# Kernel optimization log

Measured on AMD Instinct MI355X. Metric: run time of the kernel, lower is better.

The kernel has to match this reference:

```python
import jax, jax.numpy as jnp
import numpy as np

N_QUBITS = 10
DIM = 2 ** N_QUBITS
N_TOKENS = 32
LAYERS = 2
DEGREE = 3
VOCAB = 32000
EMB = 512
N_PARAMS = 4 * N_QUBITS * LAYERS      # angles per token circuit
N_PARAMS_FF = 4 * N_QUBITS            # quantum feedforward (1 layer)
BATCH = 32


def _ry(state, wire, theta, n):
    # state: [B, 2**n] complex64; theta: [B] float32. RY = [[c,-s],[s,c]], c=cos(th/2)
    st = state.reshape(-1, 2 ** wire, 2, 2 ** (n - wire - 1))
    c = jnp.cos(theta / 2)[:, None, None]
    s = jnp.sin(theta / 2)[:, None, None]
    a, b = st[:, :, 0, :], st[:, :, 1, :]
    st = jnp.stack([c * a - s * b, s * a + c * b], axis=2)
    return st.reshape(-1, 2 ** n)


def _crx(state, ctrl, tgt, theta, n):
    # controlled-RX: apply RX=[[c,-i s],[-i s,c]] on tgt where ctrl bit == 1
    lo, hi = (ctrl, tgt) if ctrl < tgt else (tgt, ctrl)
    st = state.reshape(-1, 2 ** lo, 2, 2 ** (hi - lo - 1), 2, 2 ** (n - hi - 1))
    caxis = 2 if ctrl < tgt else 4
    taxis = 4 if ctrl < tgt else 2
    c = jnp.cos(theta / 2).reshape(-1, 1, 1, 1, 1, 1)
    s = jnp.sin(theta / 2).reshape(-1, 1, 1, 1, 1, 1)
    c0 = jax.lax.index_in_dim(st, 0, caxis, keepdims=True)
    c1 = jax.lax.index_in_dim(st, 1, caxis, keepdims=True)
    a = jax.lax.index_in_dim(c1, 0, taxis, keepdims=True)
    b = jax.lax.index_in_dim(c1, 1, taxis, keepdims=True)
    na = c * a - 1j * s * b
    nb = -1j * s * a + c * b
    c1 = jnp.concatenate([na, nb], axis=taxis)
    st = jnp.concatenate([c0, c1], axis=caxis)
    return st.reshape(-1, 2 ** n)


def _ansatz14(state, params, n, layers):
    # gate order of ansatz 14 (arXiv:1905.10876); params: [B, 4*n*layers]
    idx = 0
    for _ in range(layers):
        for i in range(n):
            state = _ry(state, i, params[:, idx], n); idx += 1
        for i in range(n - 1, -1, -1):
            state = _crx(state, i, (i + 1) % n, params[:, idx], n); idx += 1
        for i in range(n):
            state = _ry(state, i, params[:, idx], n); idx += 1
        for i in [n - 1] + list(range(n - 1)):
            state = _crx(state, i, (i - 1) % n, params[:, idx], n); idx += 1
    return state


def _measure_xyz(state, n):
    # expectation of X,Y,Z on every wire; output [B, 3*n] ordered [x..., y..., z...]
    B = state.shape[0]
    xs, ys, zs = [], [], []
    for w in range(n):
        st = state.reshape(B, 2 ** w, 2, 2 ** (n - w - 1))
        a, b = st[:, :, 0, :], st[:, :, 1, :]
        z = jnp.sum(jnp.conj(a) * b, axis=(1, 2))
        xs.append(2.0 * jnp.real(z))
        ys.append(2.0 * jnp.imag(z))
        zs.append(jnp.sum(jnp.real(a * jnp.conj(a)) - jnp.real(b * jnp.conj(b)), axis=(1, 2)))
    return jnp.stack(xs + ys + zs, axis=1)


def _forward(x, emb, w_ang, b_ang, qsvt_coeffs, lcu_re, lcu_im, qff_params, w1, b1, w2, b2):
    B, T = x.shape
    lcu = (lcu_re + 1j * lcu_im).astype(jnp.complex64)
    lcu = lcu / jnp.maximum(jnp.sum(jnp.abs(lcu)), 1e-12)          # p=1 normalize
    angles = (emb[x] @ w_ang.T + b_ang).reshape(B * T, N_PARAMS)   # [B*T, P]
    init = jnp.zeros((B, DIM), jnp.complex64).at[:, 0].set(1.0)
    acc = qsvt_coeffs[0] * init
    mono = init
    for k in range(1, DEGREE + 1):
        rep = jnp.repeat(mono, T, axis=0)                          # [B*T, D]
        st = _ansatz14(rep, angles, N_QUBITS, LAYERS).reshape(B, T, DIM)
        mono = jnp.einsum('bwi,w->bi', st, lcu)                    # LCU combine
        acc = acc + qsvt_coeffs[k] * mono
    qsvt_state = acc / jnp.sum(jnp.abs(qsvt_coeffs))
    norm = jnp.linalg.norm(qsvt_state, axis=-1, keepdims=True)
    normed = qsvt_state / jnp.maximum(norm, 1e-12)
    qff = jnp.broadcast_to(qff_params[None, :], (B, N_PARAMS_FF))
    st2 = _ansatz14(normed, qff, N_QUBITS, 1)
    ev = _measure_xyz(st2, N_QUBITS)                               # [B, 3*nq]
    h = jax.nn.relu(ev @ w1.T + b1)
    logits = h @ w2.T + b2
    return logits, jnp.mean(norm[:, 0])


def setup_inputs() -> dict:
    key = jax.random.key(0)
    ks = jax.random.split(key, 9)
    return {
        'x': jax.random.randint(ks[0], (BATCH, N_TOKENS), 0, VOCAB, dtype=jnp.int32),
        'emb': jax.random.normal(ks[1], (VOCAB, EMB), jnp.float32) * 0.02,
        'w_ang': jax.random.normal(ks[2], (N_PARAMS, EMB), jnp.float32) * (1.0 / np.sqrt(EMB)),
        'b_ang': jnp.zeros((N_PARAMS,), jnp.float32),
        'qsvt_coeffs': jax.random.uniform(ks[3], (DEGREE + 1,), jnp.float32),
        'lcu_re': jax.random.uniform(ks[4], (N_TOKENS,), jnp.float32),
        'lcu_im': jax.random.uniform(ks[5], (N_TOKENS,), jnp.float32),
        'qff_params': jax.random.uniform(ks[6], (N_PARAMS_FF,), jnp.float32),
        'w1': jax.random.normal(ks[7], (EMB, 3 * N_QUBITS), jnp.float32) * (1.0 / np.sqrt(3 * N_QUBITS)),
        'b1': jnp.zeros((EMB,), jnp.float32),
        'w2': jax.random.normal(ks[8], (VOCAB, EMB), jnp.float32) * (1.0 / np.sqrt(EMB)),
        'b2': jnp.zeros((VOCAB,), jnp.float32),
    }


def reference(x, emb, w_ang, b_ang, qsvt_coeffs, lcu_re, lcu_im, qff_params, w1, b1, w2, b2):
    return _forward(x, emb, w_ang, b_ang, qsvt_coeffs, lcu_re, lcu_im, qff_params, w1, b1, w2, b2)
```

## Files before the change

### kernel.cpp

```cpp
#include <hip/hip_runtime.h>
#include <math.h>

#define DEV __device__ __forceinline__

namespace {

struct C2 { float x, y; };

constexpr size_t OFF_CS   = 0;
constexpr size_t OFF_QFF  = 163840;
constexpr size_t OFF_LCU  = 163920;
constexpr size_t OFF_DEN  = 163984;
constexpr size_t OFF_NRM  = 163988;
constexpr size_t OFF_MONO = 164096;
constexpr size_t OFF_ACC  = 229632;
constexpr size_t OFF_ST   = 295168;
constexpr size_t OFF_EV   = 2392320;
constexpr size_t OFF_H    = 2393280;


template<int P>
DEV void ry_gate(C2 v[16], int lane, float c, float s) {
  if constexpr (P >= 6) {
    constexpr int rm = 1 << (P - 6);
#pragma unroll
    for (int r = 0; r < 16; ++r) {
      if ((r & rm) == 0) {
        C2 a = v[r], b = v[r | rm];
        v[r].x      = fmaf(c, a.x, -s * b.x);
        v[r].y      = fmaf(c, a.y, -s * b.y);
        v[r | rm].x = fmaf(s, a.x,  c * b.x);
        v[r | rm].y = fmaf(s, a.y,  c * b.y);
      }
    }
  } else {
    constexpr int lm = 1 << P;
    float sg = (lane & lm) ? s : -s;
#pragma unroll
    for (int r = 0; r < 16; ++r) {
      float px = __shfl_xor(v[r].x, lm, 64);
      float py = __shfl_xor(v[r].y, lm, 64);
      v[r].x = fmaf(c, v[r].x, sg * px);
      v[r].y = fmaf(c, v[r].y, sg * py);
    }
  }
}

template<int PC, int PT>
DEV void crx_gate(C2 v[16], int lane, float c, float s) {
  if constexpr (PT >= 6) {
    constexpr int tm = 1 << (PT - 6);
#pragma unroll
    for (int r = 0; r < 16; ++r) {
      if ((r & tm) == 0) {
        if constexpr (PC >= 6) {
          constexpr int cm = 1 << (PC - 6);
          if ((r & cm) != 0) {
            C2 a = v[r], b = v[r | tm];
            v[r].x      = fmaf(c, a.x,  s * b.y);
            v[r].y      = fmaf(c, a.y, -s * b.x);
            v[r | tm].x = fmaf(c, b.x,  s * a.y);
            v[r | tm].y = fmaf(c, b.y, -s * a.x);
          }
        } else {
          constexpr int cl = 1 << PC;
          bool ct = (lane & cl) != 0;
          C2 a = v[r], b = v[r | tm];
          float nax = fmaf(c, a.x,  s * b.y);
          float nay = fmaf(c, a.y, -s * b.x);
          float nbx = fmaf(c, b.x,  s * a.y);
          float nby = fmaf(c, b.y, -s * a.x);
          v[r].x      = ct ? nax : a.x;
          v[r].y      = ct ? nay : a.y;
          v[r | tm].x = ct ? nbx : b.x;
          v[r | tm].y = ct ? nby : b.y;
        }
      }
    }
  } else {
    constexpr int tm = 1 << PT;
#pragma unroll
    for (int r = 0; r < 16; ++r) {
      if constexpr (PC >= 6) {
        constexpr int cm = 1 << (PC - 6);
        if ((r & cm) == 0) continue;
      }
      float px = __shfl_xor(v[r].x, tm, 64);
      float py = __shfl_xor(v[r].y, tm, 64);
      float nx = fmaf(c, v[r].x,  s * py);
      float ny = fmaf(c, v[r].y, -s * px);
      if constexpr (PC >= 6) {
        v[r].x = nx; v[r].y = ny;
      } else {
        constexpr int cl = 1 << PC;
        bool ct = (lane & cl) != 0;
        v[r].x = ct ? nx : v[r].x;
        v[r].y = ct ? ny : v[r].y;
      }
    }
  }
}

#define RYG(w, g)       ry_gate<9-(w)>(v, lane, cs[2*(g)], cs[2*(g)+1])
#define CRXG(cw, tw, g) crx_gate<9-(cw), 9-(tw)>(v, lane, cs[2*(g)], cs[2*(g)+1])

DEV void apply_layer(C2 v[16], int lane, const float* __restrict__ cs) {
  RYG(0,0); RYG(1,1); RYG(2,2); RYG(3,3); RYG(4,4);
  RYG(5,5); RYG(6,6); RYG(7,7); RYG(8,8); RYG(9,9);
  CRXG(9,0,10); CRXG(8,9,11); CRXG(7,8,12); CRXG(6,7,13); CRXG(5,6,14);
  CRXG(4,5,15); CRXG(3,4,16); CRXG(2,3,17); CRXG(1,2,18); CRXG(0,1,19);
  RYG(0,20); RYG(1,21); RYG(2,22); RYG(3,23); RYG(4,24);
  RYG(5,25); RYG(6,26); RYG(7,27); RYG(8,28); RYG(9,29);
  CRXG(9,8,30); CRXG(0,9,31); CRXG(1,0,32); CRXG(2,1,33); CRXG(3,2,34);
  CRXG(4,3,35); CRXG(5,4,36); CRXG(6,5,37); CRXG(7,6,38); CRXG(8,7,39);
}

template<int P>
DEV void measure_wire(const C2 v[16], int lane, float* ev, int w) {
  float x = 0.f, y = 0.f, z = 0.f;
  if constexpr (P >= 6) {
    constexpr int rm = 1 << (P - 6);
#pragma unroll
    for (int r = 0; r < 16; ++r) {
      if ((r & rm) == 0) {
        C2 a = v[r], b = v[r | rm];
        x += a.x*b.x + a.y*b.y;
        y += a.x*b.y - a.y*b.x;
        z += (a.x*a.x + a.y*a.y) - (b.x*b.x + b.y*b.y);
      }
    }
  } else {
    constexpr int lm = 1 << P;
#pragma unroll
    for (int r = 0; r < 16; ++r) {
      float px = __shfl_xor(v[r].x, lm, 64);
      float py = __shfl_xor(v[r].y, lm, 64);
      if ((lane & lm) == 0) {
        C2 a = v[r];
        x += a.x*px + a.y*py;
        y += a.x*py - a.y*px;
        z += (a.x*a.x + a.y*a.y) - (px*px + py*py);
      }
    }
  }
  for (int s = 1; s < 64; s <<= 1) {
    x += __shfl_xor(x, s, 64);
    y += __shfl_xor(y, s, 64);
    z += __shfl_xor(z, s, 64);
  }
  if (lane == 0) {
    ev[w]      = 2.f * x;
    ev[10 + w] = 2.f * y;
    ev[20 + w] = z;
  }
}

DEV void measure_all(const C2 v[16], int lane, float* ev) {
  measure_wire<9>(v, lane, ev, 0);
  measure_wire<8>(v, lane, ev, 1);
  measure_wire<7>(v, lane, ev, 2);
  measure_wire<6>(v, lane, ev, 3);
  measure_wire<5>(v, lane, ev, 4);
  measure_wire<4>(v, lane, ev, 5);
  measure_wire<3>(v, lane, ev, 6);
  measure_wire<2>(v, lane, ev, 7);
  measure_wire<1>(v, lane, ev, 8);
  measure_wire<0>(v, lane, ev, 9);
}


__global__ void k_init(float* __restrict__ ws, const float* __restrict__ coef,
                       const float* __restrict__ lr, const float* __restrict__ li,
                       const float* __restrict__ qff) {
  if (blockIdx.x == 0 && threadIdx.x < 64) {
    int lane = threadIdx.x;
    float re = 0.f, im = 0.f;
    if (lane < 32) { re = lr[lane]; im = li[lane]; }
    float tot = sqrtf(re * re + im * im);
    for (int s = 1; s < 64; s <<= 1) tot += __shfl_xor(tot, s, 64);
    float L = fmaxf(tot, 1e-12f);
    if (lane < 32) {
      ws[OFF_LCU + 2 * lane]     = re / L;
      ws[OFF_LCU + 2 * lane + 1] = im / L;
    }
    float dv = (lane < 4) ? fabsf(coef[lane]) : 0.f;
    for (int s = 1; s < 64; s <<= 1) dv += __shfl_xor(dv, s, 64);
    if (lane == 0) ws[OFF_DEN] = dv;
    if (lane < 40) {
      float th = 0.5f * qff[lane];
      ws[OFF_QFF + 2 * lane]     = cosf(th);
      ws[OFF_QFF + 2 * lane + 1] = sinf(th);
    }
  }
  int idx = blockIdx.x * 256 + threadIdx.x;
  float c0 = coef[0];
  bool z = (idx & 1023) == 0;
  float2* mono = (float2*)(ws + OFF_MONO);
  float2* acc  = (float2*)(ws + OFF_ACC);
  mono[idx] = make_float2(z ? 1.f : 0.f, 0.f);
  acc[idx]  = make_float2(z ? c0 : 0.f, 0.f);
}

__global__ __launch_bounds__(128) void k_angles(const int* __restrict__ x,
                                                const float* __restrict__ emb,
                                                const float* __restrict__ w_ang,
                                                const float* __restrict__ b_ang,
                                                float* __restrict__ ws) {
  __shared__ float4 e4[128];
  int tok = blockIdx.x;
  int tid = threadIdx.x;
  int row = x[tok];
  e4[tid] = ((const float4*)(emb + (size_t)row * 512))[tid];
  __syncthreads();
  if (tid < 80) {
    const float4* wr = (const float4*)(w_ang + (size_t)tid * 512);
    float acc = b_ang[tid];
#pragma unroll 4
    for (int j = 0; j < 128; ++j) {
      float4 w = wr[j];
      float4 e = e4[j];
      acc = fmaf(w.x, e.x, acc);
      acc = fmaf(w.y, e.y, acc);
      acc = fmaf(w.z, e.z, acc);
      acc = fmaf(w.w, e.w, acc);
    }
    float th = 0.5f * acc;
    ws[OFF_CS + (size_t)tok * 160 + 2 * tid]     = cosf(th);
    ws[OFF_CS + (size_t)tok * 160 + 2 * tid + 1] = sinf(th);
  }
}

__global__ __launch_bounds__(256) void k_evolve(float* __restrict__ ws) {
  __shared__ float cs_lds[640];
  int tid = threadIdx.x;
  const float* csg = ws + OFF_CS + (size_t)blockIdx.x * 640;
  for (int i = tid; i < 640; i += 256) cs_lds[i] = csg[i];
  __syncthreads();
  int wid = tid >> 6, lane = tid & 63;
  int state = blockIdx.x * 4 + wid;
  int b = state >> 5, t = state & 31;
  const float2* mono = (const float2*)(ws + OFF_MONO) + (size_t)b * 1024;
  C2 v[16];
#pragma unroll
  for (int r = 0; r < 16; ++r) {
    float2 m = mono[(r << 6) | lane];
    v[r].x = m.x; v[r].y = m.y;
  }
  const float* csw = &cs_lds[wid * 160];
#pragma unroll 1
  for (int l = 0; l < 2; ++l)
    apply_layer(v, lane, csw + l * 80);
  float2 w = ((const float2*)(ws + OFF_LCU))[t];
  float2* st = (float2*)(ws + OFF_ST) + (size_t)state * 1024;
#pragma unroll
  for (int r = 0; r < 16; ++r) {
    st[(r << 6) | lane] = make_float2(w.x * v[r].x - w.y * v[r].y,
                                      w.x * v[r].y + w.y * v[r].x);
  }
}

__global__ void k_reduce(float* __restrict__ ws, const float* __restrict__ coef, int k) {
  int idx = blockIdx.x * 256 + threadIdx.x;
  int b = idx >> 10, i = idx & 1023;
  const float2* st = (const float2*)(ws + OFF_ST) + (size_t)b * 32768 + i;
  float sx = 0.f, sy = 0.f;
#pragma unroll
  for (int t = 0; t < 32; ++t) {
    float2 vv = st[t * 1024];
    sx += vv.x; sy += vv.y;
  }
  float2* mono = (float2*)(ws + OFF_MONO);
  float2* acc  = (float2*)(ws + OFF_ACC);
  mono[idx] = make_float2(sx, sy);
  float ck = coef[k];
  float2 a = acc[idx];
  a.x = fmaf(ck, sx, a.x);
  a.y = fmaf(ck, sy, a.y);
  acc[idx] = a;
}

__global__ __launch_bounds__(64) void k_final(float* __restrict__ ws) {
  int lane = threadIdx.x;
  int b = blockIdx.x;
  const float2* acc = (const float2*)(ws + OFF_ACC) + (size_t)b * 1024;
  float invd = 1.f / ws[OFF_DEN];
  C2 v[16];
  float ssum = 0.f;
#pragma unroll
  for (int r = 0; r < 16; ++r) {
    float2 m = acc[(r << 6) | lane];
    v[r].x = m.x * invd; v[r].y = m.y * invd;
    ssum += v[r].x * v[r].x + v[r].y * v[r].y;
  }
  for (int s = 1; s < 64; s <<= 1) ssum += __shfl_xor(ssum, s, 64);
  float nrm = sqrtf(ssum);
  if (lane == 0) ws[OFF_NRM + b] = nrm;
  float sc = 1.f / fmaxf(nrm, 1e-12f);
#pragma unroll
  for (int r = 0; r < 16; ++r) { v[r].x *= sc; v[r].y *= sc; }
  apply_layer(v, lane, ws + OFF_QFF);
  measure_all(v, lane, ws + OFF_EV + b * 30);
}

__global__ void k_mlp1(float* __restrict__ ws, const float* __restrict__ w1,
                       const float* __restrict__ b1, float* __restrict__ out) {
  int idx = blockIdx.x * 256 + threadIdx.x;
  int b = idx >> 9, j = idx & 511;
  const float* ev = ws + OFF_EV + b * 30;
  const float* wr = w1 + (size_t)j * 30;
  float a = b1[j];
#pragma unroll
  for (int q = 0; q < 30; ++q) a = fmaf(ev[q], wr[q], a);
  ws[OFF_H + idx] = fmaxf(a, 0.f);
  if (idx == 0) {
    float s = 0.f;
    for (int i = 0; i < 32; ++i) s += ws[OFF_NRM + i];
    out[32000u * 32u] = s * (1.f / 32.f);
  }
}

__global__ __launch_bounds__(256) void k_logits(const float* __restrict__ ws,
                                                const float* __restrict__ w2,
                                                const float* __restrict__ b2,
                                                float* __restrict__ out) {
  __shared__ float4 hT[4096];
  int tid = threadIdx.x;
  const float4* hg = (const float4*)(ws + OFF_H);
#pragma unroll
  for (int p = 0; p < 16; ++p) {
    int idx = tid + p * 256;
    int m = idx >> 7, kf4 = idx & 127;
    hT[m * 128 + (kf4 ^ (m >> 3))] = hg[idx];
  }
  __syncthreads();

  int wv = tid >> 6, lane = tid & 63;
  int mg = lane & 3, nl = lane >> 2;
  int nbase = blockIdx.x * 128;
  float acc[8][8];
#pragma unroll
  for (int j = 0; j < 8; ++j)
#pragma unroll
    for (int mi = 0; mi < 8; ++mi) acc[j][mi] = 0.f;

  const float* wbase = w2 + (size_t)(nbase + nl * 8) * 512 + wv * 128;
  int kqb = wv * 32;
  for (int kf4 = 0; kf4 < 32; ++kf4) {
    int kcol = kqb + kf4;
    float4 h4[8];
#pragma unroll
    for (int mi = 0; mi < 8; ++mi) {
      int m = mg * 8 + mi;
      h4[mi] = hT[m * 128 + (kcol ^ mg)];
    }
#pragma unroll
    for (int j = 0; j < 8; ++j) {
      float4 w4 = *(const float4*)(wbase + (size_t)j * 512 + kf4 * 4);
#pragma unroll
      for (int mi = 0; mi < 8; ++mi) {
        acc[j][mi] = fmaf(w4.x, h4[mi].x, acc[j][mi]);
        acc[j][mi] = fmaf(w4.y, h4[mi].y, acc[j][mi]);
        acc[j][mi] = fmaf(w4.z, h4[mi].z, acc[j][mi]);
        acc[j][mi] = fmaf(w4.w, h4[mi].w, acc[j][mi]);
      }
    }
  }

  __syncthreads();
  if (wv != 0) {
    int r = wv - 1;
    float4* cb = hT + r * 1024 + lane * 16;
#pragma unroll
    for (int mi = 0; mi < 8; ++mi) {
#pragma unroll
      for (int jh = 0; jh < 2; ++jh) {
        int q = mi * 2 + jh;
        float4 vv = make_float4(acc[jh*4+0][mi], acc[jh*4+1][mi],
                                acc[jh*4+2][mi], acc[jh*4+3][mi]);
        cb[q ^ (lane & 15)] = vv;
      }
    }
  }
  __syncthreads();
  if (wv == 0) {
#pragma unroll
    for (int r = 0; r < 3; ++r) {
      const float4* cb = hT + r * 1024 + lane * 16;
#pragma unroll
      for (int mi = 0; mi < 8; ++mi) {
#pragma unroll
        for (int jh = 0; jh < 2; ++jh) {
          int q = mi * 2 + jh;
          float4 vv = cb[q ^ (lane & 15)];
          acc[jh*4+0][mi] += vv.x;
          acc[jh*4+1][mi] += vv.y;
          acc[jh*4+2][mi] += vv.z;
          acc[jh*4+3][mi] += vv.w;
        }
      }
    }
    float4 b2lo = *(const float4*)(b2 + nbase + nl * 8);
    float4 b2hi = *(const float4*)(b2 + nbase + nl * 8 + 4);
#pragma unroll
    for (int mi = 0; mi < 8; ++mi) {
      int m = mg * 8 + mi;
      float* orow = out + (size_t)m * 32000 + nbase + nl * 8;
      float4 lo = make_float4(acc[0][mi] + b2lo.x, acc[1][mi] + b2lo.y,
                              acc[2][mi] + b2lo.z, acc[3][mi] + b2lo.w);
      float4 hi = make_float4(acc[4][mi] + b2hi.x, acc[5][mi] + b2hi.y,
                              acc[6][mi] + b2hi.z, acc[7][mi] + b2hi.w);
      *(float4*)(orow)     = lo;
      *(float4*)(orow + 4) = hi;
    }
  }
}

}

extern "C" void kernel_launch(void* const* d_in, const int* in_sizes, int n_in,
                              void* d_out, int out_size, void* d_ws, size_t ws_size,
                              hipStream_t stream) {
  (void)in_sizes; (void)n_in; (void)out_size; (void)ws_size;
  const int*   x    = (const int*)d_in[0];
  const float* emb  = (const float*)d_in[1];
  const float* wang = (const float*)d_in[2];
  const float* bang = (const float*)d_in[3];
  const float* coef = (const float*)d_in[4];
  const float* lre  = (const float*)d_in[5];
  const float* lim  = (const float*)d_in[6];
  const float* qff  = (const float*)d_in[7];
  const float* w1   = (const float*)d_in[8];
  const float* b1   = (const float*)d_in[9];
  const float* w2   = (const float*)d_in[10];
  const float* b2   = (const float*)d_in[11];
  float* out = (float*)d_out;
  float* ws  = (float*)d_ws;

  hipLaunchKernelGGL(k_init,   dim3(128),  dim3(256), 0, stream, ws, coef, lre, lim, qff);
  hipLaunchKernelGGL(k_angles, dim3(1024), dim3(128), 0, stream, x, emb, wang, bang, ws);
  for (int k = 1; k <= 3; ++k) {
    hipLaunchKernelGGL(k_evolve, dim3(256), dim3(256), 0, stream, ws);
    hipLaunchKernelGGL(k_reduce, dim3(128), dim3(256), 0, stream, ws, coef, k);
  }
  hipLaunchKernelGGL(k_final,  dim3(32),   dim3(64),  0, stream, ws);
  hipLaunchKernelGGL(k_mlp1,   dim3(64),   dim3(256), 0, stream, ws, w1, b1, out);
  hipLaunchKernelGGL(k_logits, dim3(250),  dim3(256), 0, stream, ws, w2, b2, out);
}
```

Baseline: 162.2 us.

## Fuse whole pipeline into one cooperative persistent kernel with grid syncs

Replaces ten separate kernel launches with a single cooperative kernel of 256 blocks that uses grid-wide syncs between stages. Angles for each block's four tokens are computed straight into shared memory instead of going through global memory. The first monomial state is built in registers, and the QSVT accumulator is kept in registers across iterations. The aim is to remove launch gaps and intermediate global traffic, at the cost of grid-sync overhead and the occupancy limits of a cooperative launch.

New measurement: 386.8 us. 138% more time.

```diff
diff --git a/kernel.cpp b/kernel.cpp
--- a/kernel.cpp
+++ b/kernel.cpp
@@ -1,16 +1,15 @@
 #include <hip/hip_runtime.h>
+#include <hip/hip_cooperative_groups.h>
 #include <math.h>
 
+namespace cg = cooperative_groups;
+
 #define DEV __device__ __forceinline__
 
 namespace {
 
 struct C2 { float x, y; };
 
-constexpr size_t OFF_CS   = 0;
-constexpr size_t OFF_QFF  = 163840;
-constexpr size_t OFF_LCU  = 163920;
-constexpr size_t OFF_DEN  = 163984;
 constexpr size_t OFF_NRM  = 163988;
 constexpr size_t OFF_MONO = 164096;
 constexpr size_t OFF_ACC  = 229632;
@@ -168,249 +167,277 @@
   measure_wire<0>(v, lane, ev, 9);
 }
 
-
-__global__ void k_init(float* __restrict__ ws, const float* __restrict__ coef,
-                       const float* __restrict__ lr, const float* __restrict__ li,
-                       const float* __restrict__ qff) {
-  if (blockIdx.x == 0 && threadIdx.x < 64) {
-    int lane = threadIdx.x;
-    float re = 0.f, im = 0.f;
-    if (lane < 32) { re = lr[lane]; im = li[lane]; }
-    float tot = sqrtf(re * re + im * im);
-    for (int s = 1; s < 64; s <<= 1) tot += __shfl_xor(tot, s, 64);
-    float L = fmaxf(tot, 1e-12f);
-    if (lane < 32) {
-      ws[OFF_LCU + 2 * lane]     = re / L;
-      ws[OFF_LCU + 2 * lane + 1] = im / L;
-    }
-    float dv = (lane < 4) ? fabsf(coef[lane]) : 0.f;
-    for (int s = 1; s < 64; s <<= 1) dv += __shfl_xor(dv, s, 64);
-    if (lane == 0) ws[OFF_DEN] = dv;
-    if (lane < 40) {
-      float th = 0.5f * qff[lane];
-      ws[OFF_QFF + 2 * lane]     = cosf(th);
-      ws[OFF_QFF + 2 * lane + 1] = sinf(th);
-    }
-  }
-  int idx = blockIdx.x * 256 + threadIdx.x;
-  float c0 = coef[0];
-  bool z = (idx & 1023) == 0;
-  float2* mono = (float2*)(ws + OFF_MONO);
-  float2* acc  = (float2*)(ws + OFF_ACC);
-  mono[idx] = make_float2(z ? 1.f : 0.f, 0.f);
-  acc[idx]  = make_float2(z ? c0 : 0.f, 0.f);
-}
-
-__global__ __launch_bounds__(128) void k_angles(const int* __restrict__ x,
-                                                const float* __restrict__ emb,
-                                                const float* __restrict__ w_ang,
-                                                const float* __restrict__ b_ang,
-                                                float* __restrict__ ws) {
-  __shared__ float4 e4[128];
-  int tok = blockIdx.x;
-  int tid = threadIdx.x;
-  int row = x[tok];
-  e4[tid] = ((const float4*)(emb + (size_t)row * 512))[tid];
-  __syncthreads();
-  if (tid < 80) {
-    const float4* wr = (const float4*)(w_ang + (size_t)tid * 512);
-    float acc = b_ang[tid];
+__global__ __launch_bounds__(256) void k_mega(
+    const int* __restrict__ x, const float* __restrict__ emb,
+    const float* __restrict__ w_ang, const float* __restrict__ b_ang,
+    const float* __restrict__ coef, const float* __restrict__ lr,
+    const float* __restrict__ li, const float* __restrict__ qff,
+    const float* __restrict__ w1, const float* __restrict__ b1,
+    const float* __restrict__ w2, const float* __restrict__ b2,
+    float* __restrict__ out, float* __restrict__ ws) {
+  cg::grid_group grid = cg::this_grid();
+
+  __shared__ float4 hT[4096];
+  __shared__ float  cs_lds[4][160];
+  __shared__ float  qff_lds[80];
+
+  const int tid  = threadIdx.x;
+  const int g    = blockIdx.x;
+  const int wid  = tid >> 6;
+  const int lane = tid & 63;
+
+  float lre_v = 0.f, lim_v = 0.f;
+  if (lane < 32) { lre_v = lr[lane]; lim_v = li[lane]; }
+  float ab = sqrtf(lre_v * lre_v + lim_v * lim_v);
+  for (int s = 1; s < 64; s <<= 1) ab += __shfl_xor(ab, s, 64);
+  const float invL = 1.f / fmaxf(ab, 1e-12f);
+  const int state  = g * 4 + wid;
+  const int sb     = state >> 5;
+  const int stok   = state & 31;
+  const float wre = __shfl(lre_v, stok, 64) * invL;
+  const float wim = __shfl(lim_v, stok, 64) * invL;
+
+  {
+    float* e4 = (float*)hT;
+    int tok = g * 4 + wid;
+    int row = x[tok];
+    const float4* er = (const float4*)(emb + (size_t)row * 512);
+    float4* dst = (float4*)(e4 + wid * 512);
+    dst[lane]      = er[lane];
+    dst[lane + 64] = er[lane + 64];
+    __syncthreads();
+    if (tid < 80) {
+      const float4* wr = (const float4*)(w_ang + (size_t)tid * 512);
+      float bv = b_ang[tid];
+      float a0 = bv, a1 = bv, a2 = bv, a3 = bv;
+      const float4* e0p = (const float4*)(e4);
+      const float4* e1p = (const float4*)(e4 + 512);
+      const float4* e2p = (const float4*)(e4 + 1024);
+      const float4* e3p = (const float4*)(e4 + 1536);
 #pragma unroll 4
-    for (int j = 0; j < 128; ++j) {
-      float4 w = wr[j];
-      float4 e = e4[j];
-      acc = fmaf(w.x, e.x, acc);
-      acc = fmaf(w.y, e.y, acc);
-      acc = fmaf(w.z, e.z, acc);
-      acc = fmaf(w.w, e.w, acc);
-    }
-    float th = 0.5f * acc;
-    ws[OFF_CS + (size_t)tok * 160 + 2 * tid]     = cosf(th);
-    ws[OFF_CS + (size_t)tok * 160 + 2 * tid + 1] = sinf(th);
-  }
-}
-
-__global__ __launch_bounds__(256) void k_evolve(float* __restrict__ ws) {
-  __shared__ float cs_lds[640];
-  int tid = threadIdx.x;
-  const float* csg = ws + OFF_CS + (size_t)blockIdx.x * 640;
-  for (int i = tid; i < 640; i += 256) cs_lds[i] = csg[i];
-  __syncthreads();
-  int wid = tid >> 6, lane = tid & 63;
-  int state = blockIdx.x * 4 + wid;
-  int b = state >> 5, t = state & 31;
-  const float2* mono = (const float2*)(ws + OFF_MONO) + (size_t)b * 1024;
-  C2 v[16];
-#pragma unroll
-  for (int r = 0; r < 16; ++r) {
-    float2 m = mono[(r << 6) | lane];
-    v[r].x = m.x; v[r].y = m.y;
-  }
-  const float* csw = &cs_lds[wid * 160];
+      for (int j = 0; j < 128; ++j) {
+        float4 w4 = wr[j];
+        float4 e0 = e0p[j], e1 = e1p[j], e2 = e2p[j], e3 = e3p[j];
+        a0 = fmaf(w4.x, e0.x, a0); a0 = fmaf(w4.y, e0.y, a0);
+        a0 = fmaf(w4.z, e0.z, a0); a0 = fmaf(w4.w, e0.w, a0);
+        a1 = fmaf(w4.x, e1.x, a1); a1 = fmaf(w4.y, e1.y, a1);
+        a1 = fmaf(w4.z, e1.z, a1); a1 = fmaf(w4.w, e1.w, a1);
+        a2 = fmaf(w4.x, e2.x, a2); a2 = fmaf(w4.y, e2.y, a2);
+        a2 = fmaf(w4.z, e2.z, a2); a2 = fmaf(w4.w, e2.w, a2);
+        a3 = fmaf(w4.x, e3.x, a3); a3 = fmaf(w4.y, e3.y, a3);
+        a3 = fmaf(w4.z, e3.z, a3); a3 = fmaf(w4.w, e3.w, a3);
+      }
+      cs_lds[0][2*tid] = cosf(0.5f*a0); cs_lds[0][2*tid+1] = sinf(0.5f*a0);
+      cs_lds[1][2*tid] = cosf(0.5f*a1); cs_lds[1][2*tid+1] = sinf(0.5f*a1);
+      cs_lds[2][2*tid] = cosf(0.5f*a2); cs_lds[2][2*tid+1] = sinf(0.5f*a2);
+      cs_lds[3][2*tid] = cosf(0.5f*a3); cs_lds[3][2*tid+1] = sinf(0.5f*a3);
+    }
+    __syncthreads();
+  }
+
+  float2* const monog = (float2*)(ws + OFF_MONO);
+  float2* const accg  = (float2*)(ws + OFF_ACC);
+  float2* const stg   = (float2*)(ws + OFF_ST);
+  float acc_x = 0.f, acc_y = 0.f;
+
 #pragma unroll 1
-  for (int l = 0; l < 2; ++l)
-    apply_layer(v, lane, csw + l * 80);
-  float2 w = ((const float2*)(ws + OFF_LCU))[t];
-  float2* st = (float2*)(ws + OFF_ST) + (size_t)state * 1024;
-#pragma unroll
-  for (int r = 0; r < 16; ++r) {
-    st[(r << 6) | lane] = make_float2(w.x * v[r].x - w.y * v[r].y,
-                                      w.x * v[r].y + w.y * v[r].x);
-  }
-}
-
-__global__ void k_reduce(float* __restrict__ ws, const float* __restrict__ coef, int k) {
-  int idx = blockIdx.x * 256 + threadIdx.x;
-  int b = idx >> 10, i = idx & 1023;
-  const float2* st = (const float2*)(ws + OFF_ST) + (size_t)b * 32768 + i;
-  float sx = 0.f, sy = 0.f;
-#pragma unroll
-  for (int t = 0; t < 32; ++t) {
-    float2 vv = st[t * 1024];
-    sx += vv.x; sy += vv.y;
-  }
-  float2* mono = (float2*)(ws + OFF_MONO);
-  float2* acc  = (float2*)(ws + OFF_ACC);
-  mono[idx] = make_float2(sx, sy);
-  float ck = coef[k];
-  float2 a = acc[idx];
-  a.x = fmaf(ck, sx, a.x);
-  a.y = fmaf(ck, sy, a.y);
-  acc[idx] = a;
-}
-
-__global__ __launch_bounds__(64) void k_final(float* __restrict__ ws) {
-  int lane = threadIdx.x;
-  int b = blockIdx.x;
-  const float2* acc = (const float2*)(ws + OFF_ACC) + (size_t)b * 1024;
-  float invd = 1.f / ws[OFF_DEN];
-  C2 v[16];
-  float ssum = 0.f;
-#pragma unroll
-  for (int r = 0; r < 16; ++r) {
-    float2 m = acc[(r << 6) | lane];
-    v[r].x = m.x * invd; v[r].y = m.y * invd;
-    ssum += v[r].x * v[r].x + v[r].y * v[r].y;
-  }
-  for (int s = 1; s < 64; s <<= 1) ssum += __shfl_xor(ssum, s, 64);
-  float nrm = sqrtf(ssum);
-  if (lane == 0) ws[OFF_NRM + b] = nrm;
-  float sc = 1.f / fmaxf(nrm, 1e-12f);
-#pragma unroll
-  for (int r = 0; r < 16; ++r) { v[r].x *= sc; v[r].y *= sc; }
-  apply_layer(v, lane, ws + OFF_QFF);
-  measure_all(v, lane, ws + OFF_EV + b * 30);
-}
-
-__global__ void k_mlp1(float* __restrict__ ws, const float* __restrict__ w1,
-                       const float* __restrict__ b1, float* __restrict__ out) {
-  int idx = blockIdx.x * 256 + threadIdx.x;
-  int b = idx >> 9, j = idx & 511;
-  const float* ev = ws + OFF_EV + b * 30;
-  const float* wr = w1 + (size_t)j * 30;
-  float a = b1[j];
-#pragma unroll
-  for (int q = 0; q < 30; ++q) a = fmaf(ev[q], wr[q], a);
-  ws[OFF_H + idx] = fmaxf(a, 0.f);
-  if (idx == 0) {
-    float s = 0.f;
-    for (int i = 0; i < 32; ++i) s += ws[OFF_NRM + i];
-    out[32000u * 32u] = s * (1.f / 32.f);
-  }
-}
-
-__global__ __launch_bounds__(256) void k_logits(const float* __restrict__ ws,
-                                                const float* __restrict__ w2,
-                                                const float* __restrict__ b2,
-                                                float* __restrict__ out) {
-  __shared__ float4 hT[4096];
-  int tid = threadIdx.x;
-  const float4* hg = (const float4*)(ws + OFF_H);
-#pragma unroll
-  for (int p = 0; p < 16; ++p) {
-    int idx = tid + p * 256;
-    int m = idx >> 7, kf4 = idx & 127;
-    hT[m * 128 + (kf4 ^ (m >> 3))] = hg[idx];
-  }
-  __syncthreads();
-
-  int wv = tid >> 6, lane = tid & 63;
-  int mg = lane & 3, nl = lane >> 2;
-  int nbase = blockIdx.x * 128;
-  float acc[8][8];
-#pragma unroll
-  for (int j = 0; j < 8; ++j)
-#pragma unroll
-    for (int mi = 0; mi < 8; ++mi) acc[j][mi] = 0.f;
-
-  const float* wbase = w2 + (size_t)(nbase + nl * 8) * 512 + wv * 128;
-  int kqb = wv * 32;
-  for (int kf4 = 0; kf4 < 32; ++kf4) {
-    int kcol = kqb + kf4;
-    float4 h4[8];
-#pragma unroll
-    for (int mi = 0; mi < 8; ++mi) {
-      int m = mg * 8 + mi;
-      h4[mi] = hT[m * 128 + (kcol ^ mg)];
-    }
-#pragma unroll
-    for (int j = 0; j < 8; ++j) {
-      float4 w4 = *(const float4*)(wbase + (size_t)j * 512 + kf4 * 4);
+  for (int k = 1; k <= 3; ++k) {
+    {
+      C2 v[16];
+      if (k == 1) {
+#pragma unroll
+        for (int r = 0; r < 16; ++r) {
+          v[r].x = (r == 0 && lane == 0) ? 1.f : 0.f;
+          v[r].y = 0.f;
+        }
+      } else {
+        const float2* mono = monog + (size_t)sb * 1024;
+#pragma unroll
+        for (int r = 0; r < 16; ++r) {
+          float2 m = mono[(r << 6) | lane];
+          v[r].x = m.x; v[r].y = m.y;
+        }
+      }
+      const float* cs0 = cs_lds[wid];
+      apply_layer(v, lane, cs0);
+      apply_layer(v, lane, cs0 + 80);
+      float2* stp = stg + (size_t)state * 1024;
+#pragma unroll
+      for (int r = 0; r < 16; ++r) {
+        stp[(r << 6) | lane] = make_float2(wre * v[r].x - wim * v[r].y,
+                                           wre * v[r].y + wim * v[r].x);
+      }
+    }
+    grid.sync();
+
+    {
+      int idx = g * 256 + tid;
+      if (idx < 32768) {
+        int b = idx >> 10, i = idx & 1023;
+        const float2* st = stg + (size_t)b * 32768 + i;
+        float sx = 0.f, sy = 0.f;
+#pragma unroll
+        for (int t = 0; t < 32; ++t) {
+          float2 vv = st[t * 1024];
+          sx += vv.x; sy += vv.y;
+        }
+        float ck = coef[k];
+        if (k == 1) {
+          float e0 = (i == 0) ? coef[0] : 0.f;
+          acc_x = e0 + ck * sx;
+          acc_y = ck * sy;
+        } else {
+          acc_x = fmaf(ck, sx, acc_x);
+          acc_y = fmaf(ck, sy, acc_y);
+        }
+        if (k < 3) {
+          monog[idx] = make_float2(sx, sy);
+        } else {
+          accg[idx] = make_float2(acc_x, acc_y);
+        }
+      }
+    }
+    grid.sync();
+  }
+
+  if (g < 32) {
+    if (tid < 40) {
+      float th = 0.5f * qff[tid];
+      qff_lds[2*tid]     = cosf(th);
+      qff_lds[2*tid + 1] = sinf(th);
+    }
+    __syncthreads();
+    if (wid == 0) {
+      float den = fabsf(coef[0]) + fabsf(coef[1]) + fabsf(coef[2]) + fabsf(coef[3]);
+      float invd = 1.f / den;
+      const float2* accp = accg + (size_t)g * 1024;
+      C2 v[16];
+      float ssum = 0.f;
+#pragma unroll
+      for (int r = 0; r < 16; ++r) {
+        float2 m = accp[(r << 6) | lane];
+        v[r].x = m.x * invd; v[r].y = m.y * invd;
+        ssum += v[r].x * v[r].x + v[r].y * v[r].y;
+      }
+      for (int s = 1; s < 64; s <<= 1) ssum += __shfl_xor(ssum, s, 64);
+      float nrm = sqrtf(ssum);
+      if (lane == 0) ws[OFF_NRM + g] = nrm;
+      float sc = 1.f / fmaxf(nrm, 1e-12f);
+#pragma unroll
+      for (int r = 0; r < 16; ++r) { v[r].x *= sc; v[r].y *= sc; }
+      apply_layer(v, lane, qff_lds);
+      measure_all(v, lane, ws + OFF_EV + g * 30);
+    }
+  }
+  grid.sync();
+
+  {
+    int idx = g * 256 + tid;
+    if (idx < 16384) {
+      int b = idx >> 9, j = idx & 511;
+      const float* ev = ws + OFF_EV + b * 30;
+      const float* wr = w1 + (size_t)j * 30;
+      float a = b1[j];
+#pragma unroll
+      for (int q = 0; q < 30; ++q) a = fmaf(ev[q], wr[q], a);
+      ws[OFF_H + idx] = fmaxf(a, 0.f);
+    }
+    if (idx == 0) {
+      float s = 0.f;
+      for (int i = 0; i < 32; ++i) s += ws[OFF_NRM + i];
+      out[32000u * 32u] = s * (1.f / 32.f);
+    }
+  }
+  grid.sync();
+
+  if (g < 250) {
+    const float4* hg = (const float4*)(ws + OFF_H);
+#pragma unroll
+    for (int p = 0; p < 16; ++p) {
+      int idx = tid + p * 256;
+      int m = idx >> 7, kf4 = idx & 127;
+      hT[m * 128 + (kf4 ^ (m >> 3))] = hg[idx];
+    }
+    __syncthreads();
+
+    int wv = wid;
+    int mg = lane & 3, nl = lane >> 2;
+    int nbase = g * 128;
+    float acc[8][8];
+#pragma unroll
+    for (int j = 0; j < 8; ++j)
+#pragma unroll
+      for (int mi = 0; mi < 8; ++mi) acc[j][mi] = 0.f;
+
+    const float* wbase = w2 + (size_t)(nbase + nl * 8) * 512 + wv * 128;
+    int kqb = wv * 32;
+    for (int kf4 = 0; kf4 < 32; ++kf4) {
+      int kcol = kqb + kf4;
+      float4 h4[8];
 #pragma unroll
       for (int mi = 0; mi < 8; ++mi) {
-        acc[j][mi] = fmaf(w4.x, h4[mi].x, acc[j][mi]);
-        acc[j][mi] = fmaf(w4.y, h4[mi].y, acc[j][mi]);
-        acc[j][mi] = fmaf(w4.z, h4[mi].z, acc[j][mi]);
-        acc[j][mi] = fmaf(w4.w, h4[mi].w, acc[j][mi]);
-      }
-    }
-  }
-
-  __syncthreads();
-  if (wv != 0) {
-    int r = wv - 1;
-    float4* cb = hT + r * 1024 + lane * 16;
-#pragma unroll
-    for (int mi = 0; mi < 8; ++mi) {
-#pragma unroll
-      for (int jh = 0; jh < 2; ++jh) {
-        int q = mi * 2 + jh;
-        float4 vv = make_float4(acc[jh*4+0][mi], acc[jh*4+1][mi],
-                                acc[jh*4+2][mi], acc[jh*4+3][mi]);
-        cb[q ^ (lane & 15)] = vv;
-      }
-    }
-  }
-  __syncthreads();
-  if (wv == 0) {
-#pragma unroll
-    for (int r = 0; r < 3; ++r) {
-      const float4* cb = hT + r * 1024 + lane * 16;
+        int m = mg * 8 + mi;
+        h4[mi] = hT[m * 128 + (kcol ^ mg)];
+      }
+#pragma unroll
+      for (int j = 0; j < 8; ++j) {
+        float4 w4 = *(const float4*)(wbase + (size_t)j * 512 + kf4 * 4);
+#pragma unroll
+        for (int mi = 0; mi < 8; ++mi) {
+          acc[j][mi] = fmaf(w4.x, h4[mi].x, acc[j][mi]);
+          acc[j][mi] = fmaf(w4.y, h4[mi].y, acc[j][mi]);
+          acc[j][mi] = fmaf(w4.z, h4[mi].z, acc[j][mi]);
+          acc[j][mi] = fmaf(w4.w, h4[mi].w, acc[j][mi]);
+        }
+      }
+    }
+
+    __syncthreads();
+    if (wv != 0) {
+      int r = wv - 1;
+      float4* cb = hT + r * 1024 + lane * 16;
 #pragma unroll
       for (int mi = 0; mi < 8; ++mi) {
 #pragma unroll
         for (int jh = 0; jh < 2; ++jh) {
           int q = mi * 2 + jh;
-          float4 vv = cb[q ^ (lane & 15)];
-          acc[jh*4+0][mi] += vv.x;
-          acc[jh*4+1][mi] += vv.y;
-          acc[jh*4+2][mi] += vv.z;
-          acc[jh*4+3][mi] += vv.w;
-        }
-      }
-    }
-    float4 b2lo = *(const float4*)(b2 + nbase + nl * 8);
-    float4 b2hi = *(const float4*)(b2 + nbase + nl * 8 + 4);
-#pragma unroll
-    for (int mi = 0; mi < 8; ++mi) {
-      int m = mg * 8 + mi;
-      float* orow = out + (size_t)m * 32000 + nbase + nl * 8;
-      float4 lo = make_float4(acc[0][mi] + b2lo.x, acc[1][mi] + b2lo.y,
-                              acc[2][mi] + b2lo.z, acc[3][mi] + b2lo.w);
-      float4 hi = make_float4(acc[4][mi] + b2hi.x, acc[5][mi] + b2hi.y,
-                              acc[6][mi] + b2hi.z, acc[7][mi] + b2hi.w);
-      *(float4*)(orow)     = lo;
-      *(float4*)(orow + 4) = hi;
+          float4 vv = make_float4(acc[jh*4+0][mi], acc[jh*4+1][mi],
+                                  acc[jh*4+2][mi], acc[jh*4+3][mi]);
+          cb[q ^ (lane & 15)] = vv;
+        }
+      }
+    }
+    __syncthreads();
+    if (wv == 0) {
+#pragma unroll
+      for (int r = 0; r < 3; ++r) {
+        const float4* cb = hT + r * 1024 + lane * 16;
+#pragma unroll
+        for (int mi = 0; mi < 8; ++mi) {
+#pragma unroll
+          for (int jh = 0; jh < 2; ++jh) {
+            int q = mi * 2 + jh;
+            float4 vv = cb[q ^ (lane & 15)];
+            acc[jh*4+0][mi] += vv.x;
+            acc[jh*4+1][mi] += vv.y;
+            acc[jh*4+2][mi] += vv.z;
+            acc[jh*4+3][mi] += vv.w;
+          }
+        }
+      }
+      float4 b2lo = *(const float4*)(b2 + nbase + nl * 8);
+      float4 b2hi = *(const float4*)(b2 + nbase + nl * 8 + 4);
+#pragma unroll
+      for (int mi = 0; mi < 8; ++mi) {
+        int m = mg * 8 + mi;
+        float* orow = out + (size_t)m * 32000 + nbase + nl * 8;
+        float4 lo = make_float4(acc[0][mi] + b2lo.x, acc[1][mi] + b2lo.y,
+                                acc[2][mi] + b2lo.z, acc[3][mi] + b2lo.w);
+        float4 hi = make_float4(acc[4][mi] + b2hi.x, acc[5][mi] + b2hi.y,
+                                acc[6][mi] + b2hi.z, acc[7][mi] + b2hi.w);
+        *(float4*)(orow)     = lo;
+        *(float4*)(orow + 4) = hi;
+      }
     }
   }
 }
@@ -436,13 +463,9 @@
   float* out = (float*)d_out;
   float* ws  = (float*)d_ws;
 
-  hipLaunchKernelGGL(k_init,   dim3(128),  dim3(256), 0, stream, ws, coef, lre, lim, qff);
-  hipLaunchKernelGGL(k_angles, dim3(1024), dim3(128), 0, stream, x, emb, wang, bang, ws);
-  for (int k = 1; k <= 3; ++k) {
-    hipLaunchKernelGGL(k_evolve, dim3(256), dim3(256), 0, stream, ws);
-    hipLaunchKernelGGL(k_reduce, dim3(128), dim3(256), 0, stream, ws, coef, k);
-  }
-  hipLaunchKernelGGL(k_final,  dim3(32),   dim3(64),  0, stream, ws);
-  hipLaunchKernelGGL(k_mlp1,   dim3(64),   dim3(256), 0, stream, ws, w1, b1, out);
-  hipLaunchKernelGGL(k_logits, dim3(250),  dim3(256), 0, stream, ws, w2, b2, out);
-}
+  void* args[] = {(void*)&x,   (void*)&emb, (void*)&wang, (void*)&bang,
+                  (void*)&coef, (void*)&lre, (void*)&lim,  (void*)&qff,
+                  (void*)&w1,  (void*)&b1,  (void*)&w2,   (void*)&b2,
+                  (void*)&out, (void*)&ws};
+  hipLaunchCooperativeKernel((void*)k_mega, dim3(256), dim3(256), args, 0, stream);
+}
```

## Fuse init, final and MLP1 kernels and batch two tokens per angle block

Applied to the files above, without the earlier changes.

Removes the separate init kernel by computing the LCU normalisation, the QSVT denominator and the qff cos/sin inside the consumers, and seeds the first evolve with the basis state directly. It merges the final measurement with the first MLP layer through shared memory and moves the mean-norm write into the logits kernel. The angle kernel now handles two tokens per block so each w_ang row load is reused twice. Together these cut three launches and some global round trips, at the cost of redundant per-wave LCU reductions in every evolve block.

Result: no change. 164.0 us (+1.1%).

```diff
diff --git a/kernel.cpp b/kernel.cpp
--- a/kernel.cpp
+++ b/kernel.cpp
@@ -8,14 +8,10 @@
 struct C2 { float x, y; };
 
 constexpr size_t OFF_CS   = 0;
-constexpr size_t OFF_QFF  = 163840;
-constexpr size_t OFF_LCU  = 163920;
-constexpr size_t OFF_DEN  = 163984;
 constexpr size_t OFF_NRM  = 163988;
 constexpr size_t OFF_MONO = 164096;
 constexpr size_t OFF_ACC  = 229632;
 constexpr size_t OFF_ST   = 295168;
-constexpr size_t OFF_EV   = 2392320;
 constexpr size_t OFF_H    = 2393280;
 
 
@@ -169,68 +165,43 @@
 }
 
 
-__global__ void k_init(float* __restrict__ ws, const float* __restrict__ coef,
-                       const float* __restrict__ lr, const float* __restrict__ li,
-                       const float* __restrict__ qff) {
-  if (blockIdx.x == 0 && threadIdx.x < 64) {
-    int lane = threadIdx.x;
-    float re = 0.f, im = 0.f;
-    if (lane < 32) { re = lr[lane]; im = li[lane]; }
-    float tot = sqrtf(re * re + im * im);
-    for (int s = 1; s < 64; s <<= 1) tot += __shfl_xor(tot, s, 64);
-    float L = fmaxf(tot, 1e-12f);
-    if (lane < 32) {
-      ws[OFF_LCU + 2 * lane]     = re / L;
-      ws[OFF_LCU + 2 * lane + 1] = im / L;
-    }
-    float dv = (lane < 4) ? fabsf(coef[lane]) : 0.f;
-    for (int s = 1; s < 64; s <<= 1) dv += __shfl_xor(dv, s, 64);
-    if (lane == 0) ws[OFF_DEN] = dv;
-    if (lane < 40) {
-      float th = 0.5f * qff[lane];
-      ws[OFF_QFF + 2 * lane]     = cosf(th);
-      ws[OFF_QFF + 2 * lane + 1] = sinf(th);
-    }
-  }
-  int idx = blockIdx.x * 256 + threadIdx.x;
-  float c0 = coef[0];
-  bool z = (idx & 1023) == 0;
-  float2* mono = (float2*)(ws + OFF_MONO);
-  float2* acc  = (float2*)(ws + OFF_ACC);
-  mono[idx] = make_float2(z ? 1.f : 0.f, 0.f);
-  acc[idx]  = make_float2(z ? c0 : 0.f, 0.f);
-}
-
 __global__ __launch_bounds__(128) void k_angles(const int* __restrict__ x,
                                                 const float* __restrict__ emb,
                                                 const float* __restrict__ w_ang,
                                                 const float* __restrict__ b_ang,
                                                 float* __restrict__ ws) {
-  __shared__ float4 e4[128];
-  int tok = blockIdx.x;
+  __shared__ float4 e2[2][128];
+  int g = blockIdx.x;
   int tid = threadIdx.x;
-  int row = x[tok];
-  e4[tid] = ((const float4*)(emb + (size_t)row * 512))[tid];
+  int r0 = x[2 * g], r1 = x[2 * g + 1];
+  e2[0][tid] = ((const float4*)(emb + (size_t)r0 * 512))[tid];
+  e2[1][tid] = ((const float4*)(emb + (size_t)r1 * 512))[tid];
   __syncthreads();
   if (tid < 80) {
     const float4* wr = (const float4*)(w_ang + (size_t)tid * 512);
-    float acc = b_ang[tid];
+    float bv = b_ang[tid];
+    float a0 = bv, a1 = bv;
 #pragma unroll 4
     for (int j = 0; j < 128; ++j) {
       float4 w = wr[j];
-      float4 e = e4[j];
-      acc = fmaf(w.x, e.x, acc);
-      acc = fmaf(w.y, e.y, acc);
-      acc = fmaf(w.z, e.z, acc);
-      acc = fmaf(w.w, e.w, acc);
-    }
-    float th = 0.5f * acc;
-    ws[OFF_CS + (size_t)tok * 160 + 2 * tid]     = cosf(th);
-    ws[OFF_CS + (size_t)tok * 160 + 2 * tid + 1] = sinf(th);
-  }
-}
-
-__global__ __launch_bounds__(256) void k_evolve(float* __restrict__ ws) {
+      float4 e0 = e2[0][j], e1 = e2[1][j];
+      a0 = fmaf(w.x, e0.x, a0); a0 = fmaf(w.y, e0.y, a0);
+      a0 = fmaf(w.z, e0.z, a0); a0 = fmaf(w.w, e0.w, a0);
+      a1 = fmaf(w.x, e1.x, a1); a1 = fmaf(w.y, e1.y, a1);
+      a1 = fmaf(w.z, e1.z, a1); a1 = fmaf(w.w, e1.w, a1);
+    }
+    float t0 = 0.5f * a0, t1 = 0.5f * a1;
+    ws[OFF_CS + (size_t)(2 * g) * 160 + 2 * tid]         = cosf(t0);
+    ws[OFF_CS + (size_t)(2 * g) * 160 + 2 * tid + 1]     = sinf(t0);
+    ws[OFF_CS + (size_t)(2 * g + 1) * 160 + 2 * tid]     = cosf(t1);
+    ws[OFF_CS + (size_t)(2 * g + 1) * 160 + 2 * tid + 1] = sinf(t1);
+  }
+}
+
+__global__ __launch_bounds__(256) void k_evolve(float* __restrict__ ws,
+                                                const float* __restrict__ lr,
+                                                const float* __restrict__ li,
+                                                int k) {
   __shared__ float cs_lds[640];
   int tid = threadIdx.x;
   const float* csg = ws + OFF_CS + (size_t)blockIdx.x * 640;
@@ -239,23 +210,38 @@
   int wid = tid >> 6, lane = tid & 63;
   int state = blockIdx.x * 4 + wid;
   int b = state >> 5, t = state & 31;
-  const float2* mono = (const float2*)(ws + OFF_MONO) + (size_t)b * 1024;
+
+  float lre_v = 0.f, lim_v = 0.f;
+  if (lane < 32) { lre_v = lr[lane]; lim_v = li[lane]; }
+  float ab = sqrtf(lre_v * lre_v + lim_v * lim_v);
+  for (int s = 1; s < 64; s <<= 1) ab += __shfl_xor(ab, s, 64);
+  float invL = 1.f / fmaxf(ab, 1e-12f);
+  float wre = __shfl(lre_v, t, 64) * invL;
+  float wim = __shfl(lim_v, t, 64) * invL;
+
   C2 v[16];
+  if (k == 1) {
+#pragma unroll
+    for (int r = 0; r < 16; ++r) {
+      v[r].x = (r == 0 && lane == 0) ? 1.f : 0.f;
+      v[r].y = 0.f;
+    }
+  } else {
+    const float2* mono = (const float2*)(ws + OFF_MONO) + (size_t)b * 1024;
+#pragma unroll
+    for (int r = 0; r < 16; ++r) {
+      float2 m = mono[(r << 6) | lane];
+      v[r].x = m.x; v[r].y = m.y;
+    }
+  }
+  const float* csw = &cs_lds[wid * 160];
+  apply_layer(v, lane, csw);
+  apply_layer(v, lane, csw + 80);
+  float2* st = (float2*)(ws + OFF_ST) + (size_t)state * 1024;
 #pragma unroll
   for (int r = 0; r < 16; ++r) {
-    float2 m = mono[(r << 6) | lane];
-    v[r].x = m.x; v[r].y = m.y;
-  }
-  const float* csw = &cs_lds[wid * 160];
-#pragma unroll 1
-  for (int l = 0; l < 2; ++l)
-    apply_layer(v, lane, csw + l * 80);
-  float2 w = ((const float2*)(ws + OFF_LCU))[t];
-  float2* st = (float2*)(ws + OFF_ST) + (size_t)state * 1024;
-#pragma unroll
-  for (int r = 0; r < 16; ++r) {
-    st[(r << 6) | lane] = make_float2(w.x * v[r].x - w.y * v[r].y,
-                                      w.x * v[r].y + w.y * v[r].x);
+    st[(r << 6) | lane] = make_float2(wre * v[r].x - wim * v[r].y,
+                                      wre * v[r].y + wim * v[r].x);
   }
 }
 
@@ -271,51 +257,66 @@
   }
   float2* mono = (float2*)(ws + OFF_MONO);
   float2* acc  = (float2*)(ws + OFF_ACC);
-  mono[idx] = make_float2(sx, sy);
   float ck = coef[k];
-  float2 a = acc[idx];
-  a.x = fmaf(ck, sx, a.x);
-  a.y = fmaf(ck, sy, a.y);
-  acc[idx] = a;
-}
-
-__global__ __launch_bounds__(64) void k_final(float* __restrict__ ws) {
-  int lane = threadIdx.x;
+  if (k == 1) {
+    float e0 = (i == 0) ? coef[0] : 0.f;
+    acc[idx] = make_float2(fmaf(ck, sx, e0), ck * sy);
+    mono[idx] = make_float2(sx, sy);
+  } else {
+    float2 a = acc[idx];
+    a.x = fmaf(ck, sx, a.x);
+    a.y = fmaf(ck, sy, a.y);
+    acc[idx] = a;
+    if (k < 3) mono[idx] = make_float2(sx, sy);
+  }
+}
+
+__global__ __launch_bounds__(256) void k_final(float* __restrict__ ws,
+                                               const float* __restrict__ coef,
+                                               const float* __restrict__ qff,
+                                               const float* __restrict__ w1,
+                                               const float* __restrict__ b1) {
+  __shared__ float qff_lds[80];
+  __shared__ float ev_lds[30];
+  int tid = threadIdx.x;
   int b = blockIdx.x;
-  const float2* acc = (const float2*)(ws + OFF_ACC) + (size_t)b * 1024;
-  float invd = 1.f / ws[OFF_DEN];
-  C2 v[16];
-  float ssum = 0.f;
-#pragma unroll
-  for (int r = 0; r < 16; ++r) {
-    float2 m = acc[(r << 6) | lane];
-    v[r].x = m.x * invd; v[r].y = m.y * invd;
-    ssum += v[r].x * v[r].x + v[r].y * v[r].y;
-  }
-  for (int s = 1; s < 64; s <<= 1) ssum += __shfl_xor(ssum, s, 64);
-  float nrm = sqrtf(ssum);
-  if (lane == 0) ws[OFF_NRM + b] = nrm;
-  float sc = 1.f / fmaxf(nrm, 1e-12f);
-#pragma unroll
-  for (int r = 0; r < 16; ++r) { v[r].x *= sc; v[r].y *= sc; }
-  apply_layer(v, lane, ws + OFF_QFF);
-  measure_all(v, lane, ws + OFF_EV + b * 30);
-}
-
-__global__ void k_mlp1(float* __restrict__ ws, const float* __restrict__ w1,
-                       const float* __restrict__ b1, float* __restrict__ out) {
-  int idx = blockIdx.x * 256 + threadIdx.x;
-  int b = idx >> 9, j = idx & 511;
-  const float* ev = ws + OFF_EV + b * 30;
-  const float* wr = w1 + (size_t)j * 30;
-  float a = b1[j];
-#pragma unroll
-  for (int q = 0; q < 30; ++q) a = fmaf(ev[q], wr[q], a);
-  ws[OFF_H + idx] = fmaxf(a, 0.f);
-  if (idx == 0) {
-    float s = 0.f;
-    for (int i = 0; i < 32; ++i) s += ws[OFF_NRM + i];
-    out[32000u * 32u] = s * (1.f / 32.f);
+  if (tid < 40) {
+    float th = 0.5f * qff[tid];
+    qff_lds[2 * tid]     = cosf(th);
+    qff_lds[2 * tid + 1] = sinf(th);
+  }
+  __syncthreads();
+  if (tid < 64) {
+    int lane = tid;
+    float den = fabsf(coef[0]) + fabsf(coef[1]) + fabsf(coef[2]) + fabsf(coef[3]);
+    float invd = 1.f / den;
+    const float2* accp = (const float2*)(ws + OFF_ACC) + (size_t)b * 1024;
+    C2 v[16];
+    float ssum = 0.f;
+#pragma unroll
+    for (int r = 0; r < 16; ++r) {
+      float2 m = accp[(r << 6) | lane];
+      v[r].x = m.x * invd; v[r].y = m.y * invd;
+      ssum += v[r].x * v[r].x + v[r].y * v[r].y;
+    }
+    for (int s = 1; s < 64; s <<= 1) ssum += __shfl_xor(ssum, s, 64);
+    float nrm = sqrtf(ssum);
+    if (lane == 0) ws[OFF_NRM + b] = nrm;
+    float sc = 1.f / fmaxf(nrm, 1e-12f);
+#pragma unroll
+    for (int r = 0; r < 16; ++r) { v[r].x *= sc; v[r].y *= sc; }
+    apply_layer(v, lane, qff_lds);
+    measure_all(v, lane, ev_lds);
+  }
+  __syncthreads();
+#pragma unroll
+  for (int jj = 0; jj < 2; ++jj) {
+    int j = tid + jj * 256;
+    const float* wr = w1 + (size_t)j * 30;
+    float a = b1[j];
+#pragma unroll
+    for (int q = 0; q < 30; ++q) a = fmaf(ev_lds[q], wr[q], a);
+    ws[OFF_H + b * 512 + j] = fmaxf(a, 0.f);
   }
 }
 
@@ -325,6 +326,11 @@
                                                 float* __restrict__ out) {
   __shared__ float4 hT[4096];
   int tid = threadIdx.x;
+  if (blockIdx.x == 0 && tid == 0) {
+    float s = 0.f;
+    for (int i = 0; i < 32; ++i) s += ws[OFF_NRM + i];
+    out[32000u * 32u] = s * (1.f / 32.f);
+  }
   const float4* hg = (const float4*)(ws + OFF_H);
 #pragma unroll
   for (int p = 0; p < 16; ++p) {
@@ -436,13 +442,11 @@
   float* out = (float*)d_out;
   float* ws  = (float*)d_ws;
 
-  hipLaunchKernelGGL(k_init,   dim3(128),  dim3(256), 0, stream, ws, coef, lre, lim, qff);
-  hipLaunchKernelGGL(k_angles, dim3(1024), dim3(128), 0, stream, x, emb, wang, bang, ws);
+  hipLaunchKernelGGL(k_angles, dim3(512), dim3(128), 0, stream, x, emb, wang, bang, ws);
   for (int k = 1; k <= 3; ++k) {
-    hipLaunchKernelGGL(k_evolve, dim3(256), dim3(256), 0, stream, ws);
+    hipLaunchKernelGGL(k_evolve, dim3(256), dim3(256), 0, stream, ws, lre, lim, k);
     hipLaunchKernelGGL(k_reduce, dim3(128), dim3(256), 0, stream, ws, coef, k);
   }
-  hipLaunchKernelGGL(k_final,  dim3(32),   dim3(64),  0, stream, ws);
-  hipLaunchKernelGGL(k_mlp1,   dim3(64),   dim3(256), 0, stream, ws, w1, b1, out);
-  hipLaunchKernelGGL(k_logits, dim3(250),  dim3(256), 0, stream, ws, w2, b2, out);
-}
+  hipLaunchKernelGGL(k_final,  dim3(32),  dim3(256), 0, stream, ws, coef, qff, w1, b1);
+  hipLaunchKernelGGL(k_logits, dim3(250), dim3(256), 0, stream, ws, w2, b2, out);
+}
```
